# Kernel optimization log

Measured on AMD Instinct MI355X. Metric: run time of the kernel, lower is better.

The kernel has to match this reference:

```python
import jax, jax.numpy as jnp
import numpy as np

D_MODEL = 1024
N_HEADS = 16
D_HEAD = D_MODEL // N_HEADS
HIDDEN = 4096
B, T = 2, 2048
EPS = 1e-5


def setup_inputs() -> dict:
    key = jax.random.key(0)
    ks = jax.random.split(key, 16)
    s = 0.02
    return {
        "x": jax.random.normal(ks[0], (B, T, D_MODEL), dtype=jnp.float32),
        # LayerNorm 1
        "gamma1": jnp.ones((D_MODEL,), jnp.float32),
        "beta1": jnp.zeros((D_MODEL,), jnp.float32),
        # attention projections, stored (in, out) so y = x @ W + b
        "Wq": jax.random.normal(ks[1], (D_MODEL, D_MODEL), jnp.float32) * s,
        "bq": jnp.zeros((D_MODEL,), jnp.float32),
        "Wk": jax.random.normal(ks[2], (D_MODEL, D_MODEL), jnp.float32) * s,
        "bk": jnp.zeros((D_MODEL,), jnp.float32),
        "Wv": jax.random.normal(ks[3], (D_MODEL, D_MODEL), jnp.float32) * s,
        "bv": jnp.zeros((D_MODEL,), jnp.float32),
        "Wo": jax.random.normal(ks[4], (D_MODEL, D_MODEL), jnp.float32) * s,
        "bo": jnp.zeros((D_MODEL,), jnp.float32),
        # LayerNorm 2
        "gamma2": jnp.ones((D_MODEL,), jnp.float32),
        "beta2": jnp.zeros((D_MODEL,), jnp.float32),
        # MLP
        "W1": jax.random.normal(ks[5], (D_MODEL, HIDDEN), jnp.float32) * s,
        "b1": jnp.zeros((HIDDEN,), jnp.float32),
        "W2": jax.random.normal(ks[6], (HIDDEN, D_MODEL), jnp.float32) * s,
        "b2": jnp.zeros((D_MODEL,), jnp.float32),
    }


def _layernorm(x, gamma, beta):
    mean = jnp.mean(x, axis=-1, keepdims=True)
    var = jnp.mean(jnp.square(x - mean), axis=-1, keepdims=True)  # unbiased=False
    return gamma * (x - mean) * jax.lax.rsqrt(var + EPS) + beta


def _attention(x, Wq, bq, Wk, bk, Wv, bv, Wo, bo):
    b, t, _ = x.shape
    q = (x @ Wq + bq).reshape(b, t, N_HEADS, D_HEAD)
    k = (x @ Wk + bk).reshape(b, t, N_HEADS, D_HEAD)
    v = (x @ Wv + bv).reshape(b, t, N_HEADS, D_HEAD)
    scores = jnp.einsum("bqhd,bkhd->bhqk", q, k) / np.sqrt(D_HEAD).astype(np.float32)
    causal = jnp.tril(jnp.ones((t, t), dtype=bool))  # keep j <= i
    scores = jnp.where(causal, scores, -jnp.inf)
    attn = jax.nn.softmax(scores, axis=-1)
    out = jnp.einsum("bhqk,bkhd->bqhd", attn, v).reshape(b, t, D_MODEL)
    return out @ Wo + bo


def reference(x, gamma1, beta1, Wq, bq, Wk, bk, Wv, bv, Wo, bo,
              gamma2, beta2, W1, b1, W2, b2):
    # x = x + Attn(LN1(x))
    x = x + _attention(_layernorm(x, gamma1, beta1), Wq, bq, Wk, bk, Wv, bv, Wo, bo)
    # x = x + MLP(LN2(x)); torch F.gelu default = exact erf gelu
    h = _layernorm(x, gamma2, beta2)
    h = jax.nn.gelu(h @ W1 + b1, approximate=False) @ W2 + b2
    return x + h
```

## Files before the change

### kernel.cpp

```cpp
#include <hip/hip_runtime.h>
#include <stdint.h>

typedef unsigned short u16;
typedef short bf16x8 __attribute__((ext_vector_type(8)));
typedef float f32x4 __attribute__((ext_vector_type(4)));
typedef float f32x16 __attribute__((ext_vector_type(16)));

#define MB (1024L*1024L)

__device__ inline u16 f2bf(float f) {
  union { float f; unsigned u; } v; v.f = f;
  unsigned r = (v.u + 0x7FFFu + ((v.u >> 16) & 1u)) >> 16;
  return (u16)r;
}

__device__ inline float bf2f(u16 u) {
  union { unsigned u; float f; } v; v.u = ((unsigned)u) << 16; return v.f;
}

__device__ inline unsigned cvtpk(float lo, float hi) {
  unsigned r;
  asm("v_cvt_pk_bf16_f32 %0, %1, %2" : "=v"(r) : "v"(lo), "v"(hi));
  return r;
}

#define GLOAD16(gptr, lptr) \
  __builtin_amdgcn_global_load_lds((__attribute__((address_space(1))) void*)(gptr), \
                                   (__attribute__((address_space(3))) void*)(lptr), 16, 0, 0)

__global__ __launch_bounds__(256) void wprep(
    const float* __restrict__ Wq, const float* __restrict__ Wk,
    const float* __restrict__ Wv, const float* __restrict__ Wo,
    const float* __restrict__ W1, const float* __restrict__ W2,
    const float* __restrict__ bq, const float* __restrict__ bk,
    const float* __restrict__ bv,
    u16* __restrict__ WqkvT, u16* __restrict__ WoT,
    u16* __restrict__ W1T, u16* __restrict__ W2T, float* __restrict__ bqkv,
    const float* __restrict__ x, const float* __restrict__ gamma1,
    const float* __restrict__ beta1, u16* __restrict__ xn) {
  const int blk = blockIdx.x;
  const int tid = threadIdx.x;
  __shared__ float tile[32][33];
  __shared__ float red[8];

  if (blk >= 12292) {
    const int row = blk - 12292;
    const float4 v = *(const float4*)(x + (size_t)row * 1024 + tid * 4);
    float s = v.x + v.y + v.z + v.w;
    float s2 = v.x * v.x + v.y * v.y + v.z * v.z + v.w * v.w;
#pragma unroll
    for (int mm = 1; mm < 64; mm <<= 1) {
      s += __shfl_xor(s, mm, 64);
      s2 += __shfl_xor(s2, mm, 64);
    }
    const int w = tid >> 6;
    if ((tid & 63) == 0) { red[w] = s; red[4 + w] = s2; }
    __syncthreads();
    s = red[0] + red[1] + red[2] + red[3];
    s2 = red[4] + red[5] + red[6] + red[7];
    const float mean = s * (1.0f / 1024.0f);
    const float var = s2 * (1.0f / 1024.0f) - mean * mean;
    const float rstd = rsqrtf(var + 1e-5f);
    const float4 g = *(const float4*)(gamma1 + tid * 4);
    const float4 bb = *(const float4*)(beta1 + tid * 4);
    ushort4 o;
    o.x = f2bf(g.x * (v.x - mean) * rstd + bb.x);
    o.y = f2bf(g.y * (v.y - mean) * rstd + bb.y);
    o.z = f2bf(g.z * (v.z - mean) * rstd + bb.z);
    o.w = f2bf(g.w * (v.w - mean) * rstd + bb.w);
    *(ushort4*)(xn + (size_t)row * 1024 + tid * 4) = o;
    return;
  }
  if (blk >= 12288) {
    int i = (blk - 12288) * 256 + tid;
    bqkv[i] = bq[i]; bqkv[1024 + i] = bk[i]; bqkv[2048 + i] = bv[i];
    return;
  }
  const float* W; u16* WT; int K, N, tb;
  if (blk < 4096) {
    K = 1024; N = 1024;
    if (blk < 1024)      { W = Wq; WT = WqkvT;               tb = blk; }
    else if (blk < 2048) { W = Wk; WT = WqkvT + 1024 * 1024; tb = blk - 1024; }
    else if (blk < 3072) { W = Wv; WT = WqkvT + 2048 * 1024; tb = blk - 2048; }
    else                 { W = Wo; WT = WoT;                 tb = blk - 3072; }
  } else if (blk < 8192) { W = W1; WT = W1T; K = 1024; N = 4096; tb = blk - 4096; }
  else                   { W = W2; WT = W2T; K = 4096; N = 1024; tb = blk - 8192; }

  const int nbn = N >> 5;
  const int bk_ = tb / nbn;
  const int bn = tb % nbn;
  const int r = tid >> 3;
  const int c4 = (tid & 7) << 2;
  const float4 v = *(const float4*)(W + (size_t)(bk_ * 32 + r) * N + bn * 32 + c4);
  tile[r][c4 + 0] = v.x; tile[r][c4 + 1] = v.y;
  tile[r][c4 + 2] = v.z; tile[r][c4 + 3] = v.w;
  __syncthreads();
  ushort4 o;
  o.x = f2bf(tile[c4 + 0][r]); o.y = f2bf(tile[c4 + 1][r]);
  o.z = f2bf(tile[c4 + 2][r]); o.w = f2bf(tile[c4 + 3][r]);
  *(ushort4*)(WT + (size_t)(bn * 32 + r) * K + bk_ * 32 + c4) = o;
}

__global__ __launch_bounds__(256) void ln_kernel(const float* __restrict__ x,
                                                 const float* __restrict__ gamma,
                                                 const float* __restrict__ beta,
                                                 u16* __restrict__ out) {
  const int row = blockIdx.x;
  const int tid = threadIdx.x;
  const float4 v = *(const float4*)(x + (size_t)row * 1024 + tid * 4);
  float s = v.x + v.y + v.z + v.w;
  float s2 = v.x * v.x + v.y * v.y + v.z * v.z + v.w * v.w;
#pragma unroll
  for (int m = 1; m < 64; m <<= 1) {
    s += __shfl_xor(s, m, 64);
    s2 += __shfl_xor(s2, m, 64);
  }
  __shared__ float red[8];
  const int w = tid >> 6;
  if ((tid & 63) == 0) { red[w] = s; red[4 + w] = s2; }
  __syncthreads();
  s = red[0] + red[1] + red[2] + red[3];
  s2 = red[4] + red[5] + red[6] + red[7];
  const float mean = s * (1.0f / 1024.0f);
  const float var = s2 * (1.0f / 1024.0f) - mean * mean;
  const float rstd = rsqrtf(var + 1e-5f);
  const float4 g = *(const float4*)(gamma + tid * 4);
  const float4 b = *(const float4*)(beta + tid * 4);
  ushort4 o;
  o.x = f2bf(g.x * (v.x - mean) * rstd + b.x);
  o.y = f2bf(g.y * (v.y - mean) * rstd + b.y);
  o.z = f2bf(g.z * (v.z - mean) * rstd + b.z);
  o.w = f2bf(g.w * (v.w - mean) * rstd + b.w);
  *(ushort4*)(out + (size_t)row * 1024 + tid * 4) = o;
}

template <int EPI>
__global__ __launch_bounds__(512, 1)
void gemm256sq(const u16* __restrict__ A, const u16* __restrict__ BT,
               const float* __restrict__ bias, void* __restrict__ outp,
               int M, int N, int K) {
  __shared__ __align__(16) u16 As[2][256 * 64];
  __shared__ __align__(16) u16 Bs[2][256 * 64];
  const int nBN = N >> 8;
  const int blk = blockIdx.x;
  const int xcd = blk & 7;
  const int rr = blk >> 3;
  const int bm = xcd * 2 + rr / nBN;
  const int bn = rr % nBN;
  const int tid = threadIdx.x;
  const int lane = tid & 63;
  const int wid = tid >> 6;
  const int wm = wid >> 2;
  const int wn = wid & 3;
  const int e4 = lane >> 4;
  const int l15 = lane & 15;
  const int sx = l15 & 7;

  const int aoffb = (wm * 128 + l15) * 64;
  const int boffb = (wn * 64 + l15) * 64;
  const int ch0 = ((e4 ^ sx) & 7) << 3;
  const int ch1 = (((4 | e4) ^ sx) & 7) << 3;

  size_t gA[2], gB[2]; int lo[2];
#pragma unroll
  for (int c = 0; c < 2; ++c) {
    int idx = tid + (c << 9);
    int rowl = idx >> 3;
    int chg = ((idx & 7) ^ (rowl & 7)) << 3;
    gA[c] = (size_t)(bm * 256 + rowl) * K + chg;
    gB[c] = (size_t)(bn * 256 + rowl) * K + chg;
    lo[c] = idx << 4;
  }
  const size_t hK = (size_t)128 * K;

#define STG_A(tt, h) do { _Pragma("unroll") for (int c = 0; c < 2; ++c) \
  GLOAD16(A + gA[c] + (size_t)(h) * hK + (size_t)(tt) * 64, (char*)As[(tt) & 1] + (h) * 16384 + lo[c]); } while (0)
#define STG_B(tt, h) do { _Pragma("unroll") for (int c = 0; c < 2; ++c) \
  GLOAD16(BT + gB[c] + (size_t)(h) * hK + (size_t)(tt) * 64, (char*)Bs[(tt) & 1] + (h) * 16384 + lo[c]); } while (0)

  f32x4 acc[8][4] = {};
  const int nt = K >> 6;

  STG_A(0, 0); STG_A(0, 1); STG_B(0, 0); STG_B(0, 1);
  STG_B(1, 0); STG_B(1, 1);
  asm volatile("s_waitcnt vmcnt(4)" ::: "memory");
  __builtin_amdgcn_s_barrier();

  for (int t = 0; t < nt; ++t) {
    const u16* Ap = As[t & 1];
    const u16* Bp = Bs[t & 1];
    bf16x8 a[2][4], b01[2][2], b23[2][2];

#pragma unroll
    for (int mm = 0; mm < 4; ++mm) {
      a[0][mm] = *(const bf16x8*)(Ap + aoffb + mm * 1024 + ch0);
      a[1][mm] = *(const bf16x8*)(Ap + aoffb + mm * 1024 + ch1);
    }
#pragma unroll
    for (int nn = 0; nn < 2; ++nn) {
      b01[0][nn] = *(const bf16x8*)(Bp + boffb + nn * 1024 + ch0);
      b01[1][nn] = *(const bf16x8*)(Bp + boffb + nn * 1024 + ch1);
    }
    if (t + 1 < nt) STG_A(t + 1, 0);
    __builtin_amdgcn_s_barrier();
    asm volatile("s_waitcnt lgkmcnt(0)" ::: "memory");
    __builtin_amdgcn_s_setprio(1);
#pragma unroll
    for (int kk = 0; kk < 2; ++kk)
#pragma unroll
      for (int mm = 0; mm < 4; ++mm)
#pragma unroll
        for (int nn = 0; nn < 2; ++nn)
          acc[mm][nn] = __builtin_amdgcn_mfma_f32_16x16x32_bf16(a[kk][mm], b01[kk][nn], acc[mm][nn], 0, 0, 0);
    __builtin_amdgcn_s_setprio(0);
    __builtin_amdgcn_s_barrier();

#pragma unroll
    for (int nn = 0; nn < 2; ++nn) {
      b23[0][nn] = *(const bf16x8*)(Bp + boffb + (2 + nn) * 1024 + ch0);
      b23[1][nn] = *(const bf16x8*)(Bp + boffb + (2 + nn) * 1024 + ch1);
    }
    if (t + 1 < nt) STG_A(t + 1, 1);
    __builtin_amdgcn_s_barrier();
    asm volatile("s_waitcnt lgkmcnt(0)" ::: "memory");
    __builtin_amdgcn_s_setprio(1);
#pragma unroll
    for (int kk = 0; kk < 2; ++kk)
#pragma unroll
      for (int mm = 0; mm < 4; ++mm)
#pragma unroll
        for (int nn = 0; nn < 2; ++nn)
          acc[mm][2 + nn] = __builtin_amdgcn_mfma_f32_16x16x32_bf16(a[kk][mm], b23[kk][nn], acc[mm][2 + nn], 0, 0, 0);
    __builtin_amdgcn_s_setprio(0);
    __builtin_amdgcn_s_barrier();

#pragma unroll
    for (int mm = 0; mm < 4; ++mm) {
      a[0][mm] = *(const bf16x8*)(Ap + aoffb + (4 + mm) * 1024 + ch0);
      a[1][mm] = *(const bf16x8*)(Ap + aoffb + (4 + mm) * 1024 + ch1);
    }
    if (t + 2 < nt) STG_B(t + 2, 0);
    __builtin_amdgcn_s_barrier();
    asm volatile("s_waitcnt lgkmcnt(0)" ::: "memory");
    __builtin_amdgcn_s_setprio(1);
#pragma unroll
    for (int kk = 0; kk < 2; ++kk)
#pragma unroll
      for (int mm = 0; mm < 4; ++mm)
#pragma unroll
        for (int nn = 0; nn < 2; ++nn)
          acc[4 + mm][2 + nn] = __builtin_amdgcn_mfma_f32_16x16x32_bf16(a[kk][mm], b23[kk][nn], acc[4 + mm][2 + nn], 0, 0, 0);
    __builtin_amdgcn_s_setprio(0);
    __builtin_amdgcn_s_barrier();

    if (t + 2 < nt) STG_B(t + 2, 1);
    __builtin_amdgcn_s_barrier();
    __builtin_amdgcn_s_setprio(1);
#pragma unroll
    for (int kk = 0; kk < 2; ++kk)
#pragma unroll
      for (int mm = 0; mm < 4; ++mm)
#pragma unroll
        for (int nn = 0; nn < 2; ++nn)
          acc[4 + mm][nn] = __builtin_amdgcn_mfma_f32_16x16x32_bf16(a[kk][mm], b01[kk][nn], acc[4 + mm][nn], 0, 0, 0);
    __builtin_amdgcn_s_setprio(0);
    if (t + 1 < nt) {
      if (t + 2 < nt) asm volatile("s_waitcnt vmcnt(4)" ::: "memory");
      else            asm volatile("s_waitcnt vmcnt(0)" ::: "memory");
    }
    __builtin_amdgcn_s_barrier();
  }
#undef STG_A
#undef STG_B

  const int rbase = bm * 256 + wm * 128;
  const int cbase = bn * 256 + wn * 64;
#pragma unroll
  for (int m = 0; m < 8; ++m) {
#pragma unroll
    for (int n = 0; n < 4; ++n) {
      const int col = cbase + n * 16 + l15;
      const int row0 = rbase + m * 16 + e4 * 4;
      const float bv = bias[col];
#pragma unroll
      for (int r = 0; r < 4; ++r) {
        const int row = row0 + r;
        float v = acc[m][n][r] + bv;
        if (EPI == 2) {
          float tt = v * (1.0f + 0.044715f * v * v);
          float sg = 1.0f / (1.0f + __expf(-1.5957691216057308f * tt));
          ((u16*)outp)[(size_t)row * N + col] = f2bf(v * sg);
        } else {
          ((u16*)outp)[(size_t)row * N + col] = f2bf(v);
        }
      }
    }
  }
}

template <int EPI, int BN>
__global__ __launch_bounds__(256, (BN == 64) ? 3 : 2)
void gemm_bt(const u16* __restrict__ A, const u16* __restrict__ BT,
             const float* __restrict__ bias, const float* __restrict__ res,
             void* __restrict__ outp, int M, int N, int K) {
  constexpr int MF = (BN == 128) ? 4 : 2;
  constexpr int ACH = 4;
  constexpr int BCH = BN / 32;
  constexpr int LOADS = ACH + BCH;
  __shared__ __align__(16) u16 As[2][128 * 64];
  __shared__ __align__(16) u16 Bs[2][BN * 64];
  const int nBN = N / BN;
  const int hw = blockIdx.x;
  const int xcd = hw & 7;
  const int rr = hw >> 3;
  const int bm = xcd * 4 + rr / nBN;
  const int bn = rr % nBN;
  const int tid = threadIdx.x;
  const int lane = tid & 63;
  const int wid = tid >> 6;
  const int wm = (BN == 128) ? (wid >> 1) : wid;
  const int wn = (BN == 128) ? (wid & 1) : 0;
  const int e4 = lane >> 4;

  int abase[MF], ax[MF];
#pragma unroll
  for (int m = 0; m < MF; ++m) {
    int rowa = wm * (MF * 16) + m * 16 + (lane & 15);
    abase[m] = rowa * 64; ax[m] = rowa & 7;
  }
  int bbase[4], bx[4];
#pragma unroll
  for (int n = 0; n < 4; ++n) {
    int rowb = wn * 64 + n * 16 + (lane & 15);
    bbase[n] = rowb * 64; bx[n] = rowb & 7;
  }

  size_t ga[ACH]; int loa[ACH];
#pragma unroll
  for (int c = 0; c < ACH; ++c) {
    int idx = tid + (c << 8);
    int row = idx >> 3;
    int ch = (idx & 7) ^ (row & 7);
    ga[c] = (size_t)(bm * 128 + row) * K + (ch << 3);
    loa[c] = idx << 4;
  }
  size_t gb[BCH]; int lob[BCH];
#pragma unroll
  for (int c = 0; c < BCH; ++c) {
    int idx = tid + (c << 8);
    int row = idx >> 3;
    int ch = (idx & 7) ^ (row & 7);
    gb[c] = (size_t)(bn * BN + row) * K + (ch << 3);
    lob[c] = idx << 4;
  }

#define STAGE_G(t, bb) do { \
  _Pragma("unroll") for (int c = 0; c < ACH; ++c) \
    GLOAD16(A + ga[c] + (size_t)(t) * 64, (char*)As[bb] + loa[c]); \
  _Pragma("unroll") for (int c = 0; c < BCH; ++c) \
    GLOAD16(BT + gb[c] + (size_t)(t) * 64, (char*)Bs[bb] + lob[c]); \
} while (0)

  f32x4 acc[MF][4] = {};
  const int nt = K >> 6;

  STAGE_G(0, 0);
  STAGE_G(1, 1);

  for (int t = 0; t < nt; ++t) {
    if (t + 1 < nt) {
      asm volatile("s_waitcnt vmcnt(%0)" :: "i"(LOADS) : "memory");
    } else {
      asm volatile("s_waitcnt vmcnt(0)" ::: "memory");
    }
    __builtin_amdgcn_s_barrier();
    const u16* Ap = As[t & 1];
    const u16* Bp = Bs[t & 1];
    bf16x8 af[2][MF], bfr[2][4];
#pragma unroll
    for (int kk = 0; kk < 2; ++kk) {
#pragma unroll
      for (int m = 0; m < MF; ++m)
        af[kk][m] = *(const bf16x8*)(Ap + abase[m] + (((((kk << 2) | e4)) ^ ax[m]) << 3));
#pragma unroll
      for (int n = 0; n < 4; ++n)
        bfr[kk][n] = *(const bf16x8*)(Bp + bbase[n] + (((((kk << 2) | e4)) ^ bx[n]) << 3));
    }
    asm volatile("s_waitcnt lgkmcnt(0)" ::: "memory");
    __builtin_amdgcn_s_barrier();
    if (t + 2 < nt) STAGE_G(t + 2, t & 1);
    __builtin_amdgcn_s_setprio(1);
#pragma unroll
    for (int kk = 0; kk < 2; ++kk)
#pragma unroll
      for (int m = 0; m < MF; ++m)
#pragma unroll
        for (int n = 0; n < 4; ++n)
          acc[m][n] = __builtin_amdgcn_mfma_f32_16x16x32_bf16(af[kk][m], bfr[kk][n], acc[m][n], 0, 0, 0);
    __builtin_amdgcn_s_setprio(0);
  }
#undef STAGE_G

  const int rbase = bm * 128 + wm * (MF * 16);
  const int cbase = bn * BN + wn * 64;
#pragma unroll
  for (int m = 0; m < MF; ++m) {
#pragma unroll
    for (int n = 0; n < 4; ++n) {
      const int col = cbase + n * 16 + (lane & 15);
      const int row0 = rbase + m * 16 + ((lane >> 4) << 2);
      const float bv = bias[col];
#pragma unroll
      for (int r = 0; r < 4; ++r) {
        const int row = row0 + r;
        float v = acc[m][n][r] + bv;
        if (EPI == 1) {
          ((float*)outp)[(size_t)row * N + col] = v + res[(size_t)row * N + col];
        } else if (EPI == 2) {
          float tt = v * (1.0f + 0.044715f * v * v);
          float sg = 1.0f / (1.0f + __expf(-1.5957691216057308f * tt));
          ((u16*)outp)[(size_t)row * N + col] = f2bf(v * sg);
        } else {
          ((u16*)outp)[(size_t)row * N + col] = f2bf(v);
        }
      }
    }
  }
}

__global__ __launch_bounds__(256, 2) void attn_split(const u16* __restrict__ QKV,
                                                     u16* __restrict__ Opart,
                                                     float* __restrict__ Lpart) {
  __shared__ __align__(16) u16 KV[4][4096];
  const int T = 2048, LD = 3072;
  const int blk = blockIdx.x;
  const int xcd = blk & 7;
  const int q9 = blk >> 3;
  const int bh = xcd * 4 + (q9 & 3);
  const int rest = q9 >> 2;
  const int s = rest & 1;
  const int c = 15 - (rest >> 1);
  const int b = bh >> 4, hd = bh & 15;
  const int tid = threadIdx.x;
  const int lane = tid & 63;
  const int w = tid >> 6;
  const int h = lane >> 5;
  const int qg = c * 128 + w * 32 + (lane & 31);
  const int diag = 2 * c + (w >> 1);
  const int myNt = diag + 1;
  const int ntc = 2 * c + 2;

  const u16* Qb = QKV + (size_t)b * T * LD + hd * 64;
  const u16* Kb = Qb + 1024;
  const u16* Vb = Qb + 2048;

  const float QSC = 0.18033688011112042f;
  bf16x8 qf[4];
#pragma unroll
  for (int ss = 0; ss < 4; ++ss) {
    bf16x8 raw = *(const bf16x8*)(Qb + (size_t)qg * LD + ss * 16 + h * 8);
    union { unsigned wd[4]; bf16x8 v; } u;
#pragma unroll
    for (int e = 0; e < 4; ++e)
      u.wd[e] = cvtpk(bf2f((u16)raw[2 * e]) * QSC, bf2f((u16)raw[2 * e + 1]) * QSC);
    qf[ss] = u.v;
  }

  union PF { unsigned wd[4]; bf16x8 v; } ONES;
  ONES.wd[0] = 0x3F803F80u; ONES.wd[1] = 0x3F803F80u;
  ONES.wd[2] = 0x3F803F80u; ONES.wd[3] = 0x3F803F80u;

  f32x16 NEG8;
#pragma unroll
  for (int r = 0; r < 16; ++r) NEG8[r] = -8.0f;

  f32x16 oacc[2] = {};
  f32x16 lacc = {};

  int krow[2], kgc[2], vrow[2], vcol[2];
#pragma unroll
  for (int c2 = 0; c2 < 2; ++c2) {
    int i2 = tid + (c2 << 8);
    krow[c2] = i2 >> 3;
    kgc[c2] = ((i2 & 7) ^ (krow[c2] & 7)) << 3;
    vrow[c2] = i2 >> 3;
    vcol[c2] = i2 & 7;
  }

#define VWRITE(buf, c2, vvreg) do { \
  _Pragma("unroll") for (int e = 0; e < 8; ++e) { \
    int d = vcol[c2] * 8 + e; \
    KV[2 + (buf)][(d << 6) | (vrow[c2] & 7) | ((((vrow[c2] >> 3) ^ e ^ vcol[c2]) & 7) << 3)] = (u16)(vvreg)[e]; \
  } \
} while (0)

#pragma unroll
  for (int c2 = 0; c2 < 2; ++c2) {
    GLOAD16(Kb + (size_t)(s * 64 + krow[c2]) * LD + kgc[c2], (char*)KV[0] + (tid + (c2 << 8)) * 16);
    bf16x8 vv0 = *(const bf16x8*)(Vb + (size_t)(s * 64 + vrow[c2]) * LD + vcol[c2] * 8);
    VWRITE(0, c2, vv0);
  }
  __syncthreads();

  int cur = 0;
  for (int j = s; j < ntc; j += 2) {
    const bool pre = (j + 2 < ntc);
    bf16x8 vv[2];
    if (pre) {
#pragma unroll
      for (int c2 = 0; c2 < 2; ++c2) {
        GLOAD16(Kb + (size_t)((j + 2) * 64 + krow[c2]) * LD + kgc[c2],
                (char*)KV[cur ^ 1] + (tid + (c2 << 8)) * 16);
        vv[c2] = *(const bf16x8*)(Vb + (size_t)((j + 2) * 64 + vrow[c2]) * LD + vcol[c2] * 8);
      }
    }

    if (j < myNt) {
      f32x16 sacc[2];
      const u16* Kp = KV[cur];
      __builtin_amdgcn_s_setprio(1);
#pragma unroll
      for (int t = 0; t < 2; ++t) {
        int row = t * 32 + (lane & 31);
        {
          bf16x8 kf = *(const bf16x8*)(Kp + (row << 6) + (((h ^ (row & 7)) & 7) << 3));
          sacc[t] = __builtin_amdgcn_mfma_f32_32x32x16_bf16(kf, qf[0], NEG8, 0, 0, 0);
        }
#pragma unroll
        for (int ss = 1; ss < 4; ++ss) {
          bf16x8 kf = *(const bf16x8*)(Kp + (row << 6) + ((((2 * ss + h) ^ (row & 7)) & 7) << 3));
          sacc[t] = __builtin_amdgcn_mfma_f32_32x32x16_bf16(kf, qf[ss], sacc[t], 0, 0, 0);
        }
      }
      __builtin_amdgcn_s_setprio(0);

      if (j == diag) {
#pragma unroll
        for (int t = 0; t < 2; ++t)
#pragma unroll
          for (int r = 0; r < 16; ++r) {
            int key = (j << 6) + 32 * t + (r & 3) + 8 * (r >> 2) + 4 * h;
            if (key > qg) sacc[t][r] = -200.0f;
          }
      }

#pragma unroll
      for (int t = 0; t < 2; ++t)
#pragma unroll
        for (int r = 0; r < 16; ++r)
          sacc[t][r] = exp2f(sacc[t][r]);

      union PF pf[4];
#pragma unroll
      for (int t = 0; t < 2; ++t) {
#pragma unroll
        for (int kb = 0; kb < 2; ++kb) {
          int base = 8 * kb;
          unsigned A0 = cvtpk(sacc[t][base + 0], sacc[t][base + 1]);
          unsigned A2 = cvtpk(sacc[t][base + 2], sacc[t][base + 3]);
          unsigned A4 = cvtpk(sacc[t][base + 4], sacc[t][base + 5]);
          unsigned A6 = cvtpk(sacc[t][base + 6], sacc[t][base + 7]);
          unsigned S0 = (unsigned)__shfl_xor((int)(h ? A0 : A4), 32, 64);
          unsigned S2 = (unsigned)__shfl_xor((int)(h ? A2 : A6), 32, 64);
          PF& u = pf[2 * t + kb];
          u.wd[0] = h ? S0 : A0;
          u.wd[1] = h ? S2 : A2;
          u.wd[2] = h ? A4 : S0;
          u.wd[3] = h ? A6 : S2;
        }
      }

      const u16* Vp = KV[2 + cur];
      __builtin_amdgcn_s_setprio(1);
#pragma unroll
      for (int ks = 0; ks < 4; ++ks) {
#pragma unroll
        for (int d2 = 0; d2 < 2; ++d2) {
          int d = d2 * 32 + (lane & 31);
          bf16x8 vf = *(const bf16x8*)(Vp + (d << 6) + ((((2 * ks + h) ^ (d & 7) ^ ((d >> 3) & 7)) & 7) << 3));
          oacc[d2] = __builtin_amdgcn_mfma_f32_32x32x16_bf16(vf, pf[ks].v, oacc[d2], 0, 0, 0);
        }
        lacc = __builtin_amdgcn_mfma_f32_32x32x16_bf16(ONES.v, pf[ks].v, lacc, 0, 0, 0);
      }
      __builtin_amdgcn_s_setprio(0);
    }

    if (pre) {
#pragma unroll
      for (int c2 = 0; c2 < 2; ++c2) VWRITE(cur ^ 1, c2, vv[c2]);
    }
    __syncthreads();
    cur ^= 1;
  }
#undef VWRITE

  u16* Ob = (u16*)KV;
  const int qloc = w * 32 + (lane & 31);
  if (h == 0) Lpart[(size_t)((s * 32 + bh) * 16 + c) * 128 + qloc] = lacc[0];
#pragma unroll
  for (int d2 = 0; d2 < 2; ++d2)
#pragma unroll
    for (int r = 0; r < 16; ++r) {
      int d = d2 * 32 + (r & 3) + 8 * (r >> 2) + 4 * h;
      Ob[(qloc << 6) | (d ^ ((qloc & 7) << 3))] = f2bf(oacc[d2][r]);
    }
  __syncthreads();
  const size_t pbase = (size_t)((s * 32 + bh) * 16 + c) * (128 * 64);
#pragma unroll
  for (int it = 0; it < 4; ++it) {
    int r = (tid >> 3) + it * 32;
    int c8 = tid & 7;
    bf16x8 val = *(const bf16x8*)(Ob + (r << 6) + (((c8 ^ (r & 7)) & 7) << 3));
    *(bf16x8*)(Opart + pbase + r * 64 + c8 * 8) = val;
  }
}

__global__ __launch_bounds__(256) void attn_merge(const u16* __restrict__ Opart,
                                                  const float* __restrict__ Lpart,
                                                  u16* __restrict__ O) {
  const int rowg = blockIdx.x;
  const int b = rowg >> 11;
  const int tt = rowg & 2047;
  const int c = tt >> 7;
  const int r = tt & 127;
  const int t4 = threadIdx.x;
  const int col = t4 * 4;
  const int hd = col >> 6;
  const int d0 = col & 63;
  const int bh = b * 16 + hd;
  const size_t i0 = (size_t)((0 * 32 + bh) * 16 + c) * (128 * 64) + r * 64 + d0;
  const size_t i1 = (size_t)((1 * 32 + bh) * 16 + c) * (128 * 64) + r * 64 + d0;
  const float l = Lpart[(size_t)((0 * 32 + bh) * 16 + c) * 128 + r] +
                  Lpart[(size_t)((1 * 32 + bh) * 16 + c) * 128 + r];
  const float rinv = 1.0f / l;
  ushort4 a = *(const ushort4*)(Opart + i0);
  ushort4 bb = *(const ushort4*)(Opart + i1);
  ushort4 o;
  o.x = f2bf((bf2f(a.x) + bf2f(bb.x)) * rinv);
  o.y = f2bf((bf2f(a.y) + bf2f(bb.y)) * rinv);
  o.z = f2bf((bf2f(a.z) + bf2f(bb.z)) * rinv);
  o.w = f2bf((bf2f(a.w) + bf2f(bb.w)) * rinv);
  *(ushort4*)(O + (size_t)rowg * 1024 + col) = o;
}

extern "C" void kernel_launch(void* const* d_in, const int* in_sizes, int n_in,
                              void* d_out, int out_size, void* d_ws, size_t ws_size,
                              hipStream_t stream) {
  const float* x      = (const float*)d_in[0];
  const float* gamma1 = (const float*)d_in[1];
  const float* beta1  = (const float*)d_in[2];
  const float* Wq     = (const float*)d_in[3];
  const float* bq     = (const float*)d_in[4];
  const float* Wk     = (const float*)d_in[5];
  const float* bk     = (const float*)d_in[6];
  const float* Wv     = (const float*)d_in[7];
  const float* bv     = (const float*)d_in[8];
  const float* Wo     = (const float*)d_in[9];
  const float* bo     = (const float*)d_in[10];
  const float* gamma2 = (const float*)d_in[11];
  const float* beta2  = (const float*)d_in[12];
  const float* W1     = (const float*)d_in[13];
  const float* b1     = (const float*)d_in[14];
  const float* W2     = (const float*)d_in[15];
  const float* b2     = (const float*)d_in[16];

  char* ws = (char*)d_ws;
  u16* WqkvT = (u16*)(ws + 0 * MB);
  u16* WoT   = (u16*)(ws + 6 * MB);
  u16* W1T   = (u16*)(ws + 8 * MB);
  u16* W2T   = (u16*)(ws + 16 * MB);
  u16* qkv   = (u16*)(ws + 24 * MB);
  u16* hb    = (u16*)(ws + 24 * MB);
  float* Lpart = (float*)(ws + 48 * MB);
  u16* xn    = (u16*)(ws + 56 * MB);
  float* bqkv = (float*)d_out;
  u16* Opart = (u16*)d_out;
  float* x1 = (float*)d_out;

  const int M = 4096;

  wprep<<<dim3(16388), dim3(256), 0, stream>>>(Wq, Wk, Wv, Wo, W1, W2, bq, bk, bv,
                                               WqkvT, WoT, W1T, W2T, bqkv,
                                               x, gamma1, beta1, xn);

  gemm256sq<0><<<dim3(192), dim3(512), 0, stream>>>(xn, WqkvT, bqkv, qkv, M, 3072, 1024);

  attn_split<<<dim3(1024), dim3(256), 0, stream>>>(qkv, Opart, Lpart);
  attn_merge<<<dim3(4096), dim3(256), 0, stream>>>(Opart, Lpart, xn);

  gemm_bt<1, 64><<<dim3(512), dim3(256), 0, stream>>>(xn, WoT, bo, x, x1, M, 1024, 1024);

  ln_kernel<<<dim3(M), dim3(256), 0, stream>>>(x1, gamma2, beta2, xn);

  gemm256sq<2><<<dim3(256), dim3(512), 0, stream>>>(xn, W1T, b1, hb, M, 4096, 1024);
  gemm_bt<1, 64><<<dim3(512), dim3(256), 0, stream>>>(hb, W2T, b2, x1, d_out, M, 1024, 4096);
}
```

Measured before the change: 211.5 us.

## Split-K the MLP down-projection with 256x128 tiles and a separate merge kernel

The final W2 GEMM moves from 128x64-tile blocks to a new split-K kernel. It uses 256x128 tiles and splits K into two halves across block pairs, giving 256 blocks of 512 threads with double-buffered LDS and swizzled MFMA loads. Each half writes bf16 partial sums into workspace. A new merge kernel then adds both partials, the bias and the residual in place into the output. The intent is more operand reuse per block and better CU occupancy on the long K=4096 reduction. The cost is an extra launch, an extra pass over memory for the partials, and precision loss from rounding each partial to bf16.

```diff
diff --git a/kernel.cpp b/kernel.cpp
--- a/kernel.cpp
+++ b/kernel.cpp
@@ -296,6 +296,157 @@
       }
     }
   }
+}
+
+__global__ __launch_bounds__(512, 1)
+void gemm_splitk(const u16* __restrict__ A, const u16* __restrict__ BT,
+                 u16* __restrict__ Ppart, int M, int N, int K) {
+  __shared__ __align__(16) u16 As[2][256 * 64];
+  __shared__ __align__(16) u16 Bs[2][128 * 64];
+  const int blk = blockIdx.x;
+  const int kpart = blk & 1;
+  const int tile = blk >> 1;
+  const int nBN = N >> 7;
+  const int xcd = tile & 7;
+  const int rr = tile >> 3;
+  const int bm = xcd * 2 + rr / nBN;
+  const int bn = rr % nBN;
+  const int KH = K >> 1;
+  const size_t koff = (size_t)kpart * KH;
+  const int tid = threadIdx.x;
+  const int lane = tid & 63;
+  const int wid = tid >> 6;
+  const int wm = wid >> 2;
+  const int wn = wid & 3;
+  const int e4 = lane >> 4;
+  const int l15 = lane & 15;
+  const int sx = l15 & 7;
+
+  const int aoffb = (wm * 128 + l15) * 64;
+  const int boffb = (wn * 32 + l15) * 64;
+  const int ch0 = ((e4 ^ sx) & 7) << 3;
+  const int ch1 = (((4 | e4) ^ sx) & 7) << 3;
+
+  size_t gA[4]; int loa[4];
+#pragma unroll
+  for (int c = 0; c < 4; ++c) {
+    int idx = tid + (c << 9);
+    int rowl = idx >> 3;
+    int chg = ((idx & 7) ^ (rowl & 7)) << 3;
+    gA[c] = (size_t)(bm * 256 + rowl) * K + koff + chg;
+    loa[c] = idx << 4;
+  }
+  size_t gB[2]; int lob[2];
+#pragma unroll
+  for (int c = 0; c < 2; ++c) {
+    int idx = tid + (c << 9);
+    int rowl = idx >> 3;
+    int chg = ((idx & 7) ^ (rowl & 7)) << 3;
+    gB[c] = (size_t)(bn * 128 + rowl) * K + koff + chg;
+    lob[c] = idx << 4;
+  }
+
+#define SK_A(tt, c) GLOAD16(A + gA[c] + (size_t)(tt) * 64, (char*)As[(tt) & 1] + loa[c])
+#define SK_B(tt) do { _Pragma("unroll") for (int c = 0; c < 2; ++c) \
+  GLOAD16(BT + gB[c] + (size_t)(tt) * 64, (char*)Bs[(tt) & 1] + lob[c]); } while (0)
+
+  f32x4 acc[8][2] = {};
+  const int nt = KH >> 6;
+
+  SK_A(0, 0); SK_A(0, 1); SK_A(0, 2); SK_A(0, 3);
+  SK_B(0);
+  SK_B(1);
+  asm volatile("s_waitcnt vmcnt(2)" ::: "memory");
+  __builtin_amdgcn_s_barrier();
+
+  for (int t = 0; t < nt; ++t) {
+    const u16* Ap = As[t & 1];
+    const u16* Bp = Bs[t & 1];
+    bf16x8 a[2][4], b[2][2];
+
+#pragma unroll
+    for (int mm = 0; mm < 4; ++mm) {
+      a[0][mm] = *(const bf16x8*)(Ap + aoffb + mm * 1024 + ch0);
+      a[1][mm] = *(const bf16x8*)(Ap + aoffb + mm * 1024 + ch1);
+    }
+#pragma unroll
+    for (int nn = 0; nn < 2; ++nn) {
+      b[0][nn] = *(const bf16x8*)(Bp + boffb + nn * 1024 + ch0);
+      b[1][nn] = *(const bf16x8*)(Bp + boffb + nn * 1024 + ch1);
+    }
+    if (t + 1 < nt) { SK_A(t + 1, 0); SK_A(t + 1, 1); }
+    __builtin_amdgcn_s_barrier();
+    asm volatile("s_waitcnt lgkmcnt(0)" ::: "memory");
+    __builtin_amdgcn_s_setprio(1);
+#pragma unroll
+    for (int kk = 0; kk < 2; ++kk)
+#pragma unroll
+      for (int mm = 0; mm < 4; ++mm)
+#pragma unroll
+        for (int nn = 0; nn < 2; ++nn)
+          acc[mm][nn] = __builtin_amdgcn_mfma_f32_16x16x32_bf16(a[kk][mm], b[kk][nn], acc[mm][nn], 0, 0, 0);
+    __builtin_amdgcn_s_setprio(0);
+    __builtin_amdgcn_s_barrier();
+
+#pragma unroll
+    for (int mm = 0; mm < 4; ++mm) {
+      a[0][mm] = *(const bf16x8*)(Ap + aoffb + (4 + mm) * 1024 + ch0);
+      a[1][mm] = *(const bf16x8*)(Ap + aoffb + (4 + mm) * 1024 + ch1);
+    }
+    if (t + 1 < nt) { SK_A(t + 1, 2); SK_A(t + 1, 3); }
+    if (t + 2 < nt) SK_B(t + 2);
+    __builtin_amdgcn_s_barrier();
+    asm volatile("s_waitcnt lgkmcnt(0)" ::: "memory");
+    __builtin_amdgcn_s_setprio(1);
+#pragma unroll
+    for (int kk = 0; kk < 2; ++kk)
+#pragma unroll
+      for (int mm = 0; mm < 4; ++mm)
+#pragma unroll
+        for (int nn = 0; nn < 2; ++nn)
+          acc[4 + mm][nn] = __builtin_amdgcn_mfma_f32_16x16x32_bf16(a[kk][mm], b[kk][nn], acc[4 + mm][nn], 0, 0, 0);
+    __builtin_amdgcn_s_setprio(0);
+    if (t + 1 < nt) {
+      if (t + 2 < nt) asm volatile("s_waitcnt vmcnt(2)" ::: "memory");
+      else            asm volatile("s_waitcnt vmcnt(0)" ::: "memory");
+    }
+    __builtin_amdgcn_s_barrier();
+  }
+#undef SK_A
+#undef SK_B
+
+  u16* P = Ppart + (size_t)kpart * M * N;
+  const int rbase = bm * 256 + wm * 128;
+  const int cbase = bn * 128 + wn * 32;
+#pragma unroll
+  for (int m = 0; m < 8; ++m) {
+#pragma unroll
+    for (int n = 0; n < 2; ++n) {
+      const int col = cbase + n * 16 + l15;
+      const int row0 = rbase + m * 16 + e4 * 4;
+#pragma unroll
+      for (int r = 0; r < 4; ++r)
+        P[(size_t)(row0 + r) * N + col] = f2bf(acc[m][n][r]);
+    }
+  }
+}
+
+__global__ __launch_bounds__(256) void mlp2_merge(const u16* __restrict__ Ppart,
+                                                  const float* __restrict__ b2,
+                                                  float* __restrict__ out) {
+  const int row = blockIdx.x;
+  const int col = threadIdx.x * 4;
+  const size_t base = (size_t)row * 1024 + col;
+  float4 xv = *(const float4*)(out + base);
+  float4 bb = *(const float4*)(b2 + col);
+  ushort4 p0 = *(const ushort4*)(Ppart + base);
+  ushort4 p1 = *(const ushort4*)(Ppart + (size_t)4096 * 1024 + base);
+  float4 o;
+  o.x = xv.x + bb.x + bf2f(p0.x) + bf2f(p1.x);
+  o.y = xv.y + bb.y + bf2f(p0.y) + bf2f(p1.y);
+  o.z = xv.z + bb.z + bf2f(p0.z) + bf2f(p1.z);
+  o.w = xv.w + bb.w + bf2f(p0.w) + bf2f(p1.w);
+  *(float4*)(out + base) = o;
 }
 
 template <int EPI, int BN>
@@ -673,6 +824,7 @@
   u16* hb    = (u16*)(ws + 24 * MB);
   float* Lpart = (float*)(ws + 48 * MB);
   u16* xn    = (u16*)(ws + 56 * MB);
+  u16* Ppart = (u16*)(ws + 0 * MB);
   float* bqkv = (float*)d_out;
   u16* Opart = (u16*)d_out;
   float* x1 = (float*)d_out;
@@ -693,5 +845,7 @@
   ln_kernel<<<dim3(M), dim3(256), 0, stream>>>(x1, gamma2, beta2, xn);
 
   gemm256sq<2><<<dim3(256), dim3(512), 0, stream>>>(xn, W1T, b1, hb, M, 4096, 1024);
-  gemm_bt<1, 64><<<dim3(512), dim3(256), 0, stream>>>(hb, W2T, b2, x1, d_out, M, 1024, 4096);
-}
+
+  gemm_splitk<<<dim3(256), dim3(512), 0, stream>>>(hb, W2T, Ppart, M, 1024, 4096);
+  mlp2_merge<<<dim3(4096), dim3(256), 0, stream>>>(Ppart, b2, x1);
+}
```

After: 212.1 us. Within noise of the previous version (+0.3%).
